# Performance work log

Hardware: AMD Instinct MI355X
Metric: run time of the kernel (lower is better)

## Reference

```python
import jax, jax.numpy as jnp
import numpy as np
import math

B, NQ, C = 8, 1024, 256
H, D = 8, 32            # heads, head_dim
L, P = 3, 8             # levels, points
FF = 1024
SHAPES = ((128, 128), (64, 64), (32, 32))   # (H_l, W_l) per level
STARTS = (0, 16384, 20480)
S = 21504


def _layernorm(x, w, b):
    m = x.mean(-1, keepdims=True)
    v = ((x - m) ** 2).mean(-1, keepdims=True)
    return (x - m) * jax.lax.rsqrt(v + 1e-5) * w + b


def _mha(x, in_w, in_b, out_w, out_b):
    # torch nn.MultiheadAttention self-attention, batch_first, eval (no dropout)
    qkv = x @ in_w.T + in_b                         # [B,Nq,3C]
    q, k, v = jnp.split(qkv, 3, axis=-1)
    q = q.reshape(B, NQ, H, D)
    k = k.reshape(B, NQ, H, D)
    v = v.reshape(B, NQ, H, D)
    scores = jnp.einsum('bqhd,bkhd->bhqk', q, k) / math.sqrt(D)
    attn = jax.nn.softmax(scores, axis=-1)
    o = jnp.einsum('bhqk,bkhd->bqhd', attn, v).reshape(B, NQ, C)
    return o @ out_w.T + out_b


def _msdeform(value, loc, attn_w):
    # value: [B,S,H,D]; loc: [B,Nq,H,L,P,2] in [0,1] (x,y); attn_w: [B,Nq,H,L,P]
    out = jnp.zeros((B, NQ, H, D), value.dtype)
    b_idx = jnp.arange(B)[:, None, None, None]
    h_idx = jnp.arange(H)[None, None, :, None]
    for l, (h_l, w_l) in enumerate(SHAPES):
        start = STARTS[l]
        val = value[:, start:start + h_l * w_l].reshape(B, h_l, w_l, H, D)
        # grid_sample align_corners=False unnormalization of grid=loc*2-1:
        gx = loc[:, :, :, l, :, 0] * w_l - 0.5      # [B,Nq,H,P]
        gy = loc[:, :, :, l, :, 1] * h_l - 0.5
        x0 = jnp.floor(gx); y0 = jnp.floor(gy)
        lx = gx - x0;       ly = gy - y0
        x0i = x0.astype(jnp.int32); y0i = y0.astype(jnp.int32)

        def corner(yi, xi):
            valid = ((xi >= 0) & (xi < w_l) & (yi >= 0) & (yi < h_l)).astype(value.dtype)
            xc = jnp.clip(xi, 0, w_l - 1)
            yc = jnp.clip(yi, 0, h_l - 1)
            v = val[b_idx, yc, xc, h_idx]           # [B,Nq,H,P,D]
            return v * valid[..., None]

        samp = (corner(y0i,     x0i)     * ((1 - lx) * (1 - ly))[..., None]
              + corner(y0i,     x0i + 1) * (lx * (1 - ly))[..., None]
              + corner(y0i + 1, x0i)     * ((1 - lx) * ly)[..., None]
              + corner(y0i + 1, x0i + 1) * (lx * ly)[..., None])
        out = out + (samp * attn_w[:, :, :, l, :, None]).sum(axis=3)
    return out


def _forward(tgt, memory, n1_w, n1_b, attn_in_w, attn_in_b, attn_out_w, attn_out_b,
             n2_w, n2_b, ref_w, ref_b, so_w, so_b, aw_w, aw_b, vp_w, vp_b,
             op_w, op_b, n3_w, n3_b, l1_w, l1_b, l2_w, l2_b):
    # self-attention block
    q = _layernorm(tgt, n1_w, n1_b)
    tgt = tgt + _mha(q, attn_in_w, attn_in_b, attn_out_w, attn_out_b)
    # deformable cross-attention block
    q = _layernorm(tgt, n2_w, n2_b)
    ref = jax.nn.sigmoid(q @ ref_w.T + ref_b)                                   # [B,Nq,2]
    value = (memory @ vp_w.T + vp_b).reshape(B, S, H, D)
    off = (q @ so_w.T + so_b).reshape(B, NQ, H, L, P, 2)
    aw = jax.nn.softmax((q @ aw_w.T + aw_b).reshape(B, NQ, H, L * P), axis=-1)
    aw = aw.reshape(B, NQ, H, L, P)
    normalizer = jnp.array([[w, h] for (h, w) in SHAPES], tgt.dtype)            # [L,2] (W,H)
    loc = ref[:, :, None, None, None, :] + off / normalizer[None, None, None, :, None, :]
    ca = _msdeform(value, loc, aw).reshape(B, NQ, C) @ op_w.T + op_b
    tgt = tgt + ca
    # FFN block
    q = _layernorm(tgt, n3_w, n3_b)
    ff = jax.nn.gelu(q @ l1_w.T + l1_b, approximate=False) @ l2_w.T + l2_b
    return tgt + ff


def setup_inputs() -> dict:
    key = jax.random.key(0)
    ks = jax.random.split(key, 16)
    w = lambda k, shp, s=0.02: (jax.random.normal(k, shp, jnp.float32) * s)
    # structured sampling_offsets bias (torch _reset_parameters)
    thetas = np.arange(H, dtype=np.float32) * (2.0 * math.pi / H)
    grid = np.stack([np.cos(thetas), np.sin(thetas)], -1)
    grid = grid / np.clip(np.abs(grid).max(-1, keepdims=True), 1e-6, None)
    grid = np.tile(grid.reshape(H, 1, 1, 2), (1, L, P, 1))
    grid = grid * (np.arange(P, dtype=np.float32) + 1.0).reshape(1, 1, P, 1)
    so_b = jnp.asarray(grid.reshape(-1))
    ones_c = jnp.ones((C,), jnp.float32)
    zeros_c = jnp.zeros((C,), jnp.float32)
    inp = {
        'tgt': jax.random.normal(ks[0], (B, NQ, C), jnp.float32),
        'memory': jax.random.normal(ks[1], (B, S, C), jnp.float32),
        'n1_w': ones_c, 'n1_b': zeros_c,
        'attn_in_w': w(ks[2], (3 * C, C)), 'attn_in_b': jnp.zeros((3 * C,), jnp.float32),
        'attn_out_w': w(ks[3], (C, C)), 'attn_out_b': zeros_c,
        'n2_w': ones_c, 'n2_b': zeros_c,
        'ref_w': w(ks[4], (2, C)), 'ref_b': jnp.zeros((2,), jnp.float32),
        'so_w': w(ks[5], (H * L * P * 2, C), 0.01), 'so_b': so_b,
        'aw_w': w(ks[6], (H * L * P, C)), 'aw_b': jnp.zeros((H * L * P,), jnp.float32),
        'vp_w': w(ks[7], (C, C)), 'vp_b': zeros_c,
        'op_w': w(ks[8], (C, C)), 'op_b': zeros_c,
        'n3_w': ones_c, 'n3_b': zeros_c,
        'l1_w': w(ks[9], (FF, C)), 'l1_b': jnp.zeros((FF,), jnp.float32),
        'l2_w': w(ks[10], (C, FF)), 'l2_b': zeros_c,
        'spatial_shapes': jnp.array(SHAPES, jnp.int32),
        'level_start_index': jnp.array(STARTS, jnp.int32),
    }
    return inp


def reference(tgt, memory, n1_w, n1_b, attn_in_w, attn_in_b, attn_out_w, attn_out_b,
              n2_w, n2_b, ref_w, ref_b, so_w, so_b, aw_w, aw_b, vp_w, vp_b,
              op_w, op_b, n3_w, n3_b, l1_w, l1_b, l2_w, l2_b,
              spatial_shapes, level_start_index):
    # spatial_shapes / level_start_index match the static SHAPES/STARTS constants
    return _forward(tgt, memory, n1_w, n1_b, attn_in_w, attn_in_b, attn_out_w, attn_out_b,
                    n2_w, n2_b, ref_w, ref_b, so_w, so_b, aw_w, aw_b, vp_w, vp_b,
                    op_w, op_b, n3_w, n3_b, l1_w, l1_b, l2_w, l2_b)
```

## Files before the change

### kernel.cpp

```cpp
#include <hip/hip_runtime.h>
#include <math.h>

#define NQR 1024
#define CDIM 256
#define SROWS 21504
#define ATTN_SCALE 0.17677669529663687f

typedef __attribute__((ext_vector_type(8))) short bf16x8;
typedef __attribute__((ext_vector_type(4))) float f32x4;

__device__ __forceinline__ ushort f2b(float x) {
  unsigned u = __float_as_uint(x);
  u += 0x7FFFu + ((u >> 16) & 1u);
  return (ushort)(u >> 16);
}
__device__ __forceinline__ float b2f(ushort b) {
  return __uint_as_float(((unsigned)b) << 16);
}

__global__ __launch_bounds__(256) void f2bf_kernel(
    const float* __restrict__ x, ushort* __restrict__ y) {
  int i = blockIdx.x * 256 + threadIdx.x;
  float4 v0 = ((const float4*)x)[i * 2];
  float4 v1 = ((const float4*)x)[i * 2 + 1];
  ushort4 o0, o1;
  o0.x = f2b(v0.x); o0.y = f2b(v0.y); o0.z = f2b(v0.z); o0.w = f2b(v0.w);
  o1.x = f2b(v1.x); o1.y = f2b(v1.y); o1.z = f2b(v1.z); o1.w = f2b(v1.w);
  ((ushort4*)y)[i * 2] = o0;
  ((ushort4*)y)[i * 2 + 1] = o1;
}

__global__ __launch_bounds__(256) void ln_kernel(
    const float* __restrict__ x, const float* __restrict__ w,
    const float* __restrict__ b, ushort* __restrict__ y) {
  int lane = threadIdx.x & 63;
  int row = (blockIdx.x << 2) + (threadIdx.x >> 6);
  float4 v = ((const float4*)(x + (size_t)row * CDIM))[lane];
  float s = v.x + v.y + v.z + v.w;
  float ss = v.x * v.x + v.y * v.y + v.z * v.z + v.w * v.w;
#pragma unroll
  for (int off = 32; off; off >>= 1) {
    s += __shfl_xor(s, off);
    ss += __shfl_xor(ss, off);
  }
  float m = s * (1.0f / 256.0f);
  float var = ss * (1.0f / 256.0f) - m * m;
  float r = rsqrtf(var + 1e-5f);
  float4 wv = ((const float4*)w)[lane];
  float4 bv = ((const float4*)b)[lane];
  ushort4 o;
  o.x = f2b((v.x - m) * r * wv.x + bv.x);
  o.y = f2b((v.y - m) * r * wv.y + bv.y);
  o.z = f2b((v.z - m) * r * wv.z + bv.z);
  o.w = f2b((v.w - m) * r * wv.w + bv.w);
  ((ushort4*)(y + (size_t)row * CDIM))[lane] = o;
}

template <bool GELU, bool RES, bool OUTBF>
__global__ __launch_bounds__(256) void gemm_bf16(
    const short* __restrict__ A, const short* __restrict__ W,
    const float* __restrict__ bias, const float* __restrict__ res,
    void* __restrict__ Cout, int M, int N, int K) {
  __shared__ short As[128 * 72];
  __shared__ short Bs[64 * 72];
  int t = threadIdx.x;
  int l = t & 63;
  int wave = t >> 6;
  int wm = wave >> 1, wn = wave & 1;
  int lrow = t >> 3;
  int lcol = (t & 7) << 3;
  size_t m0 = (size_t)blockIdx.x * 128;
  int n0 = blockIdx.y * 64;
  const short* Ag = A + (m0 + lrow) * K + lcol;
  const short* Wg = W + (size_t)(n0 + lrow) * K + lcol;
  f32x4 acc[4][2] = {};
  int fr = l & 15, fq = l >> 4;
  for (int k0 = 0; k0 < K; k0 += 64) {
    uint4 a0 = *(const uint4*)(Ag + k0);
    uint4 a1 = *(const uint4*)(Ag + (size_t)32 * K + k0);
    uint4 a2 = *(const uint4*)(Ag + (size_t)64 * K + k0);
    uint4 a3 = *(const uint4*)(Ag + (size_t)96 * K + k0);
    uint4 b0 = *(const uint4*)(Wg + k0);
    uint4 b1 = *(const uint4*)(Wg + (size_t)32 * K + k0);
    __syncthreads();
    *(uint4*)&As[lrow * 72 + lcol] = a0;
    *(uint4*)&As[(lrow + 32) * 72 + lcol] = a1;
    *(uint4*)&As[(lrow + 64) * 72 + lcol] = a2;
    *(uint4*)&As[(lrow + 96) * 72 + lcol] = a3;
    *(uint4*)&Bs[lrow * 72 + lcol] = b0;
    *(uint4*)&Bs[(lrow + 32) * 72 + lcol] = b1;
    __syncthreads();
#pragma unroll
    for (int kk = 0; kk < 2; kk++) {
      int kb = kk * 32 + fq * 8;
      bf16x8 af[4], bfr[2];
#pragma unroll
      for (int mi = 0; mi < 4; mi++)
        af[mi] = *(const bf16x8*)&As[(wm * 64 + mi * 16 + fr) * 72 + kb];
#pragma unroll
      for (int ni = 0; ni < 2; ni++)
        bfr[ni] = *(const bf16x8*)&Bs[(wn * 32 + ni * 16 + fr) * 72 + kb];
#pragma unroll
      for (int mi = 0; mi < 4; mi++)
#pragma unroll
        for (int ni = 0; ni < 2; ni++)
          acc[mi][ni] = __builtin_amdgcn_mfma_f32_16x16x32_bf16(
              af[mi], bfr[ni], acc[mi][ni], 0, 0, 0);
    }
  }
#pragma unroll
  for (int ni = 0; ni < 2; ni++) {
    int gcol = n0 + wn * 32 + ni * 16 + fr;
    float bv = bias[gcol];
#pragma unroll
    for (int mi = 0; mi < 4; mi++) {
#pragma unroll
      for (int j = 0; j < 4; j++) {
        size_t grow = m0 + wm * 64 + mi * 16 + fq * 4 + j;
        float v = acc[mi][ni][j] + bv;
        if (GELU) v = 0.5f * v * (1.0f + erff(v * 0.70710678118654752f));
        if (RES) v += res[grow * N + gcol];
        if (OUTBF)
          ((ushort*)Cout)[grow * N + gcol] = f2b(v);
        else
          ((float*)Cout)[grow * N + gcol] = v;
      }
    }
  }
}

__global__ __launch_bounds__(256) void attn_tiled(
    const float* __restrict__ qkv, ushort* __restrict__ o) {
  __shared__ float QsT[32][68];
  __shared__ float KsT[32][68];
  __shared__ float Vs[64][36];
  __shared__ float Ps[64][68];
  int qt = blockIdx.x;
  int bh = blockIdx.y;
  int b = bh >> 3, h = bh & 7;
  int t = threadIdx.x;
  int tx = t & 15, ty = t >> 4;
  int lr = t >> 2;
  int lc = (t & 3) << 2;

  {
    const float* qp = qkv + ((size_t)(b * NQR + qt * 64 + lr)) * 768 + h * 32;
    float4 a = *(const float4*)(qp + lc);
    float4 b4 = *(const float4*)(qp + lc + 16);
    QsT[lc + 0][lr] = a.x * ATTN_SCALE;
    QsT[lc + 1][lr] = a.y * ATTN_SCALE;
    QsT[lc + 2][lr] = a.z * ATTN_SCALE;
    QsT[lc + 3][lr] = a.w * ATTN_SCALE;
    QsT[lc + 16][lr] = b4.x * ATTN_SCALE;
    QsT[lc + 17][lr] = b4.y * ATTN_SCALE;
    QsT[lc + 18][lr] = b4.z * ATTN_SCALE;
    QsT[lc + 19][lr] = b4.w * ATTN_SCALE;
  }
  float m[4] = {-1e30f, -1e30f, -1e30f, -1e30f};
  float lsum[4] = {0.f, 0.f, 0.f, 0.f};
  float acc[4][2] = {};

  for (int kt = 0; kt < 16; kt++) {
    const float* kp = qkv + ((size_t)(b * NQR + kt * 64 + lr)) * 768 + 256 + h * 32;
    float4 k0 = *(const float4*)(kp + lc);
    float4 k1 = *(const float4*)(kp + lc + 16);
    const float* vp = kp + 256;
    float4 w0 = *(const float4*)(vp + lc);
    float4 w1 = *(const float4*)(vp + lc + 16);
    __syncthreads();
    KsT[lc + 0][lr] = k0.x;
    KsT[lc + 1][lr] = k0.y;
    KsT[lc + 2][lr] = k0.z;
    KsT[lc + 3][lr] = k0.w;
    KsT[lc + 16][lr] = k1.x;
    KsT[lc + 17][lr] = k1.y;
    KsT[lc + 18][lr] = k1.z;
    KsT[lc + 19][lr] = k1.w;
    *(float4*)&Vs[lr][lc] = w0;
    *(float4*)&Vs[lr][lc + 16] = w1;
    __syncthreads();
    float s[4][4] = {};
#pragma unroll
    for (int d = 0; d < 32; d++) {
      float4 a = *(const float4*)&QsT[d][ty << 2];
      float4 k = *(const float4*)&KsT[d][tx << 2];
      s[0][0] += a.x * k.x; s[0][1] += a.x * k.y; s[0][2] += a.x * k.z; s[0][3] += a.x * k.w;
      s[1][0] += a.y * k.x; s[1][1] += a.y * k.y; s[1][2] += a.y * k.z; s[1][3] += a.y * k.w;
      s[2][0] += a.z * k.x; s[2][1] += a.z * k.y; s[2][2] += a.z * k.z; s[2][3] += a.z * k.w;
      s[3][0] += a.w * k.x; s[3][1] += a.w * k.y; s[3][2] += a.w * k.z; s[3][3] += a.w * k.w;
    }
#pragma unroll
    for (int r = 0; r < 4; r++) {
      float mt = fmaxf(fmaxf(s[r][0], s[r][1]), fmaxf(s[r][2], s[r][3]));
      mt = fmaxf(mt, __shfl_xor(mt, 1));
      mt = fmaxf(mt, __shfl_xor(mt, 2));
      mt = fmaxf(mt, __shfl_xor(mt, 4));
      mt = fmaxf(mt, __shfl_xor(mt, 8));
      float mn = fmaxf(m[r], mt);
      float sc = __expf(m[r] - mn);
      m[r] = mn;
      float rs = 0.f;
#pragma unroll
      for (int c = 0; c < 4; c++) {
        s[r][c] = __expf(s[r][c] - mn);
        rs += s[r][c];
      }
      rs += __shfl_xor(rs, 1);
      rs += __shfl_xor(rs, 2);
      rs += __shfl_xor(rs, 4);
      rs += __shfl_xor(rs, 8);
      lsum[r] = lsum[r] * sc + rs;
      acc[r][0] *= sc;
      acc[r][1] *= sc;
      *(float4*)&Ps[(ty << 2) + r][tx << 2] = make_float4(s[r][0], s[r][1], s[r][2], s[r][3]);
    }
    __syncthreads();
#pragma unroll 4
    for (int k4 = 0; k4 < 16; k4++) {
      float pv[4][4];
#pragma unroll
      for (int r = 0; r < 4; r++) {
        float4 p4 = *(const float4*)&Ps[(ty << 2) + r][k4 << 2];
        pv[r][0] = p4.x; pv[r][1] = p4.y; pv[r][2] = p4.z; pv[r][3] = p4.w;
      }
#pragma unroll
      for (int j = 0; j < 4; j++) {
        float2 v = *(const float2*)&Vs[(k4 << 2) + j][tx << 1];
#pragma unroll
        for (int r = 0; r < 4; r++) {
          acc[r][0] += pv[r][j] * v.x;
          acc[r][1] += pv[r][j] * v.y;
        }
      }
    }
  }
  ushort* op = o + ((size_t)(b * NQR + qt * 64)) * 256 + h * 32;
#pragma unroll
  for (int r = 0; r < 4; r++) {
    float inv = 1.0f / lsum[r];
    ushort2 st;
    st.x = f2b(acc[r][0] * inv);
    st.y = f2b(acc[r][1] * inv);
    *(ushort2*)(op + (size_t)((ty << 2) + r) * 256 + (tx << 1)) = st;
  }
}

__global__ __launch_bounds__(256) void ref_kernel(
    const ushort* __restrict__ q2, const float* __restrict__ rw,
    const float* __restrict__ rb, float* __restrict__ refo) {
  int lane = threadIdx.x & 63;
  int row = (blockIdx.x << 2) + (threadIdx.x >> 6);
  ushort4 xr = ((const ushort4*)(q2 + (size_t)row * 256))[lane];
  float x0 = b2f(xr.x), x1 = b2f(xr.y), x2 = b2f(xr.z), x3 = b2f(xr.w);
  float4 w0 = ((const float4*)rw)[lane];
  float4 w1 = ((const float4*)(rw + 256))[lane];
  float d0 = x0 * w0.x + x1 * w0.y + x2 * w0.z + x3 * w0.w;
  float d1 = x0 * w1.x + x1 * w1.y + x2 * w1.z + x3 * w1.w;
#pragma unroll
  for (int off = 32; off; off >>= 1) {
    d0 += __shfl_xor(d0, off);
    d1 += __shfl_xor(d1, off);
  }
  if (lane == 0) {
    refo[row * 2 + 0] = 1.0f / (1.0f + __expf(-(d0 + rb[0])));
    refo[row * 2 + 1] = 1.0f / (1.0f + __expf(-(d1 + rb[1])));
  }
}

__global__ __launch_bounds__(256) void aw_softmax_kernel(float* __restrict__ aw) {
  int i = blockIdx.x * 256 + threadIdx.x;
  float* a = aw + (size_t)(i >> 3) * 192 + (i & 7) * 24;
  float v[24];
  float m = -1e30f;
#pragma unroll
  for (int k = 0; k < 24; k++) {
    v[k] = a[k];
    m = fmaxf(m, v[k]);
  }
  float sm = 0.f;
#pragma unroll
  for (int k = 0; k < 24; k++) {
    v[k] = __expf(v[k] - m);
    sm += v[k];
  }
  float inv = 1.0f / sm;
#pragma unroll
  for (int k = 0; k < 24; k++) a[k] = v[k] * inv;
}

__global__ __launch_bounds__(192) void msdeform_gather(
    const ushort* __restrict__ value, const float* __restrict__ ref,
    const float* __restrict__ off, const float* __restrict__ aw_n,
    float* __restrict__ lvl) {
  int q = blockIdx.x;
  int b = q >> 10;
  __shared__ float s_off[384];
  __shared__ float s_aw[192];
  int t = threadIdx.x;
#pragma unroll
  for (int i = 0; i < 3; i++) {
    int j = t + 192 * i;
    if (j < 384)
      s_off[j] = off[(size_t)q * 384 + j];
    else
      s_aw[j - 384] = aw_n[(size_t)q * 192 + (j - 384)];
  }
  __syncthreads();
  int h = t / 24;
  int rem = t - h * 24;
  int l = rem >> 3;
  int dg = rem & 7;
  int dim = (l == 0) ? 128 : ((l == 1) ? 64 : 32);
  int start = (l == 0) ? 0 : ((l == 1) ? 16384 : 20480);
  float fdim = (float)dim;
  float rx = ref[q * 2 + 0] * fdim - 0.5f;
  float ry = ref[q * 2 + 1] * fdim - 0.5f;
  const ushort* vl = value + ((size_t)b * SROWS + start) * 256 + h * 32 + dg * 4;
  int ebase = h * 24 + l * 8;
  float a0 = 0.f, a1 = 0.f, a2 = 0.f, a3 = 0.f;
#pragma unroll 2
  for (int p = 0; p < 8; p++) {
    int e = ebase + p;
    float gx = rx + s_off[e * 2];
    float gy = ry + s_off[e * 2 + 1];
    float fx = floorf(gx), fy = floorf(gy);
    int x0 = (int)fx, y0 = (int)fy;
    float lx = gx - fx, ly = gy - fy;
    float w = s_aw[e];
    bool xin0 = (x0 >= 0) & (x0 < dim);
    bool xin1 = (x0 + 1 >= 0) & (x0 + 1 < dim);
    bool yin0 = (y0 >= 0) & (y0 < dim);
    bool yin1 = (y0 + 1 >= 0) & (y0 + 1 < dim);
    ushort4 u00 = {0, 0, 0, 0}, u01 = {0, 0, 0, 0}, u10 = {0, 0, 0, 0}, u11 = {0, 0, 0, 0};
    if (yin0 && xin0) u00 = *(const ushort4*)(vl + (size_t)(y0 * dim + x0) * 256);
    if (yin0 && xin1) u01 = *(const ushort4*)(vl + (size_t)(y0 * dim + x0 + 1) * 256);
    if (yin1 && xin0) u10 = *(const ushort4*)(vl + (size_t)((y0 + 1) * dim + x0) * 256);
    if (yin1 && xin1) u11 = *(const ushort4*)(vl + (size_t)((y0 + 1) * dim + x0 + 1) * 256);
    float w00 = w * (1.f - lx) * (1.f - ly);
    float w01 = w * lx * (1.f - ly);
    float w10 = w * (1.f - lx) * ly;
    float w11 = w * lx * ly;
    a0 += b2f(u00.x) * w00 + b2f(u01.x) * w01 + b2f(u10.x) * w10 + b2f(u11.x) * w11;
    a1 += b2f(u00.y) * w00 + b2f(u01.y) * w01 + b2f(u10.y) * w10 + b2f(u11.y) * w11;
    a2 += b2f(u00.z) * w00 + b2f(u01.z) * w01 + b2f(u10.z) * w10 + b2f(u11.z) * w11;
    a3 += b2f(u00.w) * w00 + b2f(u01.w) * w01 + b2f(u10.w) * w10 + b2f(u11.w) * w11;
  }
  float4 o = make_float4(a0, a1, a2, a3);
  *(float4*)&lvl[(((size_t)q * 8 + h) * 3 + l) * 32 + dg * 4] = o;
}

__global__ __launch_bounds__(256) void msdeform_reduce(
    const float* __restrict__ lvl, ushort* __restrict__ out) {
  int t = threadIdx.x;
  int q = (blockIdx.x << 2) + (t >> 6);
  int h = (t >> 3) & 7, dg = t & 7;
  const float* p = lvl + ((size_t)q * 8 + h) * 96 + dg * 4;
  float4 x = *(const float4*)p;
  float4 y = *(const float4*)(p + 32);
  float4 z = *(const float4*)(p + 64);
  ushort4 o;
  o.x = f2b(x.x + y.x + z.x);
  o.y = f2b(x.y + y.y + z.y);
  o.z = f2b(x.z + y.z + z.z);
  o.w = f2b(x.w + y.w + z.w);
  *(ushort4*)(out + (size_t)q * 256 + h * 32 + dg * 4) = o;
}

extern "C" void kernel_launch(void* const* d_in, const int* in_sizes, int n_in,
                              void* d_out, int out_size, void* d_ws, size_t ws_size,
                              hipStream_t stream) {
  const float* tgt = (const float*)d_in[0];
  const float* memory = (const float*)d_in[1];
  const float* n1_w = (const float*)d_in[2];
  const float* n1_b = (const float*)d_in[3];
  const float* attn_in_w = (const float*)d_in[4];
  const float* attn_in_b = (const float*)d_in[5];
  const float* attn_out_w = (const float*)d_in[6];
  const float* attn_out_b = (const float*)d_in[7];
  const float* n2_w = (const float*)d_in[8];
  const float* n2_b = (const float*)d_in[9];
  const float* ref_w = (const float*)d_in[10];
  const float* ref_b = (const float*)d_in[11];
  const float* so_w = (const float*)d_in[12];
  const float* so_b = (const float*)d_in[13];
  const float* aw_w = (const float*)d_in[14];
  const float* aw_b = (const float*)d_in[15];
  const float* vp_w = (const float*)d_in[16];
  const float* vp_b = (const float*)d_in[17];
  const float* op_w = (const float*)d_in[18];
  const float* op_b = (const float*)d_in[19];
  const float* n3_w = (const float*)d_in[20];
  const float* n3_b = (const float*)d_in[21];
  const float* l1_w = (const float*)d_in[22];
  const float* l1_b = (const float*)d_in[23];
  const float* l2_w = (const float*)d_in[24];
  const float* l2_b = (const float*)d_in[25];
  float* out = (float*)d_out;

  char* base = (char*)d_ws;
  float* bufQKV = (float*)base;
  float* off_buf = (float*)(base + 25165824);
  float* aw_buf = (float*)(base + 37748736);
  float* ref_buf = (float*)(base + 44040192);
  ushort* q_bf = (ushort*)(base + 44105728);
  ushort* mha_bf = (ushort*)(base + 48300032);
  ushort* samp_bf = (ushort*)(base + 52494336);
  ushort* mem_bf = (ushort*)(base + 56688640);
  ushort* val_bf = (ushort*)(base + 144769024);
  ushort* wts = (ushort*)(base + 232849408);
  ushort* ff1_bf = (ushort*)bufQKV;
  float* lvl_buf = (float*)bufQKV;

  ushort* w_attn_in = wts;
  ushort* w_attn_out = wts + 196608;
  ushort* w_so = wts + 262144;
  ushort* w_aw = wts + 360448;
  ushort* w_vp = wts + 409600;
  ushort* w_op = wts + 475136;
  ushort* w_l1 = wts + 540672;
  ushort* w_l2 = wts + 802816;

  const int NR = 8192;

  f2bf_kernel<<<21504, 256, 0, stream>>>(memory, mem_bf);
  f2bf_kernel<<<96, 256, 0, stream>>>(attn_in_w, w_attn_in);
  f2bf_kernel<<<32, 256, 0, stream>>>(attn_out_w, w_attn_out);
  f2bf_kernel<<<48, 256, 0, stream>>>(so_w, w_so);
  f2bf_kernel<<<24, 256, 0, stream>>>(aw_w, w_aw);
  f2bf_kernel<<<32, 256, 0, stream>>>(vp_w, w_vp);
  f2bf_kernel<<<32, 256, 0, stream>>>(op_w, w_op);
  f2bf_kernel<<<128, 256, 0, stream>>>(l1_w, w_l1);
  f2bf_kernel<<<128, 256, 0, stream>>>(l2_w, w_l2);

  ln_kernel<<<NR / 4, 256, 0, stream>>>(tgt, n1_w, n1_b, q_bf);
  gemm_bf16<false, false, false><<<dim3(NR / 128, 768 / 64), 256, 0, stream>>>(
      (const short*)q_bf, (const short*)w_attn_in, attn_in_b, nullptr, bufQKV, NR, 768, 256);
  attn_tiled<<<dim3(16, 64), 256, 0, stream>>>(bufQKV, mha_bf);
  gemm_bf16<false, true, false><<<dim3(NR / 128, 256 / 64), 256, 0, stream>>>(
      (const short*)mha_bf, (const short*)w_attn_out, attn_out_b, tgt, out, NR, 256, 256);

  ln_kernel<<<NR / 4, 256, 0, stream>>>(out, n2_w, n2_b, q_bf);
  gemm_bf16<false, false, true><<<dim3(8 * SROWS / 128, 256 / 64), 256, 0, stream>>>(
      (const short*)mem_bf, (const short*)w_vp, vp_b, nullptr, val_bf, 8 * SROWS, 256, 256);
  ref_kernel<<<NR / 4, 256, 0, stream>>>(q_bf, ref_w, ref_b, ref_buf);
  gemm_bf16<false, false, false><<<dim3(NR / 128, 384 / 64), 256, 0, stream>>>(
      (const short*)q_bf, (const short*)w_so, so_b, nullptr, off_buf, NR, 384, 256);
  gemm_bf16<false, false, false><<<dim3(NR / 128, 192 / 64), 256, 0, stream>>>(
      (const short*)q_bf, (const short*)w_aw, aw_b, nullptr, aw_buf, NR, 192, 256);
  aw_softmax_kernel<<<256, 256, 0, stream>>>(aw_buf);
  msdeform_gather<<<NR, 192, 0, stream>>>(val_bf, ref_buf, off_buf, aw_buf, lvl_buf);
  msdeform_reduce<<<NR / 4, 256, 0, stream>>>(lvl_buf, samp_bf);
  gemm_bf16<false, true, false><<<dim3(NR / 128, 256 / 64), 256, 0, stream>>>(
      (const short*)samp_bf, (const short*)w_op, op_b, out, out, NR, 256, 256);

  ln_kernel<<<NR / 4, 256, 0, stream>>>(out, n3_w, n3_b, q_bf);
  gemm_bf16<true, false, true><<<dim3(NR / 128, 1024 / 64), 256, 0, stream>>>(
      (const short*)q_bf, (const short*)w_l1, l1_b, nullptr, ff1_bf, NR, 1024, 256);
  gemm_bf16<false, true, false><<<dim3(NR / 128, 256 / 64), 256, 0, stream>>>(
      (const short*)ff1_bf, (const short*)w_l2, l2_b, out, out, NR, 256, 1024);
}
```

Measured before the change: 732.8 us.

## Rewrite self-attention with bf16 MFMA and emit QKV projection in bf16

Replaces the scalar fp32 flash-attention kernel with one that computes QK^T and PV using 16x16x32 bf16 MFMA instructions. Each wave owns 16 query rows, and K and V tiles are staged in LDS, with V transposed. The QKV projection GEMM now writes bf16 instead of fp32, which halves that buffer's traffic. This moves the attention FLOPs onto matrix cores at the cost of bf16 rounding for QKV and for the probabilities.

```diff
diff --git a/kernel.cpp b/kernel.cpp
--- a/kernel.cpp
+++ b/kernel.cpp
@@ -129,119 +129,113 @@
   }
 }
 
-__global__ __launch_bounds__(256) void attn_tiled(
-    const float* __restrict__ qkv, ushort* __restrict__ o) {
-  __shared__ float QsT[32][68];
-  __shared__ float KsT[32][68];
-  __shared__ float Vs[64][36];
-  __shared__ float Ps[64][68];
-  int qt = blockIdx.x;
-  int bh = blockIdx.y;
+__global__ __launch_bounds__(256) void attn_mfma(
+    const ushort* __restrict__ qkv, ushort* __restrict__ o) {
+  __shared__ ushort Kt[64][40];
+  __shared__ ushort Vt[32][72];
+  __shared__ ushort Ps[4][16][72];
+  int qt = blockIdx.x, bh = blockIdx.y;
   int b = bh >> 3, h = bh & 7;
   int t = threadIdx.x;
-  int tx = t & 15, ty = t >> 4;
-  int lr = t >> 2;
-  int lc = (t & 3) << 2;
-
-  {
-    const float* qp = qkv + ((size_t)(b * NQR + qt * 64 + lr)) * 768 + h * 32;
-    float4 a = *(const float4*)(qp + lc);
-    float4 b4 = *(const float4*)(qp + lc + 16);
-    QsT[lc + 0][lr] = a.x * ATTN_SCALE;
-    QsT[lc + 1][lr] = a.y * ATTN_SCALE;
-    QsT[lc + 2][lr] = a.z * ATTN_SCALE;
-    QsT[lc + 3][lr] = a.w * ATTN_SCALE;
-    QsT[lc + 16][lr] = b4.x * ATTN_SCALE;
-    QsT[lc + 17][lr] = b4.y * ATTN_SCALE;
-    QsT[lc + 18][lr] = b4.z * ATTN_SCALE;
-    QsT[lc + 19][lr] = b4.w * ATTN_SCALE;
-  }
-  float m[4] = {-1e30f, -1e30f, -1e30f, -1e30f};
+  int w = t >> 6, l = t & 63;
+  int fr = l & 15, fg = l >> 4;
+
+  const ushort* qp =
+      qkv + ((size_t)(b * NQR + qt * 64 + w * 16 + fr)) * 768 + h * 32 + fg * 8;
+  bf16x8 qf = *(const bf16x8*)qp;
+
+  float mrow[4] = {-1e30f, -1e30f, -1e30f, -1e30f};
   float lsum[4] = {0.f, 0.f, 0.f, 0.f};
-  float acc[4][2] = {};
+  f32x4 accO[2] = {};
+
+  int rp = t & 31, vc = (t >> 5) & 3;
+  int tt = t & 127;
+  int krow = tt >> 1, kh = (tt & 1) * 16;
+
+  const ushort* kvbase = qkv + (size_t)b * NQR * 768 + 256 + h * 32;
 
   for (int kt = 0; kt < 16; kt++) {
-    const float* kp = qkv + ((size_t)(b * NQR + kt * 64 + lr)) * 768 + 256 + h * 32;
-    float4 k0 = *(const float4*)(kp + lc);
-    float4 k1 = *(const float4*)(kp + lc + 16);
-    const float* vp = kp + 256;
-    float4 w0 = *(const float4*)(vp + lc);
-    float4 w1 = *(const float4*)(vp + lc + 16);
+    int k0 = kt * 64;
+    uint4 ld0, ld1;
+    if (t < 128) {
+      const ushort* vp = kvbase + 256 + (size_t)(k0 + 2 * rp) * 768 + vc * 8;
+      ld0 = *(const uint4*)vp;
+      ld1 = *(const uint4*)(vp + 768);
+    } else {
+      const ushort* kp = kvbase + (size_t)(k0 + krow) * 768 + kh;
+      ld0 = *(const uint4*)kp;
+      ld1 = *(const uint4*)(kp + 8);
+    }
     __syncthreads();
-    KsT[lc + 0][lr] = k0.x;
-    KsT[lc + 1][lr] = k0.y;
-    KsT[lc + 2][lr] = k0.z;
-    KsT[lc + 3][lr] = k0.w;
-    KsT[lc + 16][lr] = k1.x;
-    KsT[lc + 17][lr] = k1.y;
-    KsT[lc + 18][lr] = k1.z;
-    KsT[lc + 19][lr] = k1.w;
-    *(float4*)&Vs[lr][lc] = w0;
-    *(float4*)&Vs[lr][lc + 16] = w1;
+    if (t < 128) {
+      ushort va[8], vb[8];
+      *(uint4*)va = ld0;
+      *(uint4*)vb = ld1;
+#pragma unroll
+      for (int j = 0; j < 8; j++) {
+        unsigned pack = (unsigned)va[j] | ((unsigned)vb[j] << 16);
+        *(unsigned*)&Vt[vc * 8 + j][2 * rp] = pack;
+      }
+    } else {
+      *(uint4*)&Kt[krow][kh] = ld0;
+      *(uint4*)&Kt[krow][kh + 8] = ld1;
+    }
     __syncthreads();
-    float s[4][4] = {};
-#pragma unroll
-    for (int d = 0; d < 32; d++) {
-      float4 a = *(const float4*)&QsT[d][ty << 2];
-      float4 k = *(const float4*)&KsT[d][tx << 2];
-      s[0][0] += a.x * k.x; s[0][1] += a.x * k.y; s[0][2] += a.x * k.z; s[0][3] += a.x * k.w;
-      s[1][0] += a.y * k.x; s[1][1] += a.y * k.y; s[1][2] += a.y * k.z; s[1][3] += a.y * k.w;
-      s[2][0] += a.z * k.x; s[2][1] += a.z * k.y; s[2][2] += a.z * k.z; s[2][3] += a.z * k.w;
-      s[3][0] += a.w * k.x; s[3][1] += a.w * k.y; s[3][2] += a.w * k.z; s[3][3] += a.w * k.w;
-    }
-#pragma unroll
-    for (int r = 0; r < 4; r++) {
-      float mt = fmaxf(fmaxf(s[r][0], s[r][1]), fmaxf(s[r][2], s[r][3]));
+    f32x4 sf[4];
+#pragma unroll
+    for (int nt = 0; nt < 4; nt++) {
+      bf16x8 kf = *(const bf16x8*)&Kt[nt * 16 + fr][fg * 8];
+      f32x4 z = {0.f, 0.f, 0.f, 0.f};
+      sf[nt] = __builtin_amdgcn_mfma_f32_16x16x32_bf16(qf, kf, z, 0, 0, 0);
+    }
+#pragma unroll
+    for (int j = 0; j < 4; j++) {
+      float s0 = sf[0][j] * ATTN_SCALE;
+      float s1 = sf[1][j] * ATTN_SCALE;
+      float s2 = sf[2][j] * ATTN_SCALE;
+      float s3 = sf[3][j] * ATTN_SCALE;
+      float mt = fmaxf(fmaxf(s0, s1), fmaxf(s2, s3));
       mt = fmaxf(mt, __shfl_xor(mt, 1));
       mt = fmaxf(mt, __shfl_xor(mt, 2));
       mt = fmaxf(mt, __shfl_xor(mt, 4));
       mt = fmaxf(mt, __shfl_xor(mt, 8));
-      float mn = fmaxf(m[r], mt);
-      float sc = __expf(m[r] - mn);
-      m[r] = mn;
-      float rs = 0.f;
-#pragma unroll
-      for (int c = 0; c < 4; c++) {
-        s[r][c] = __expf(s[r][c] - mn);
-        rs += s[r][c];
-      }
+      float mn = fmaxf(mrow[j], mt);
+      float scl = __expf(mrow[j] - mn);
+      mrow[j] = mn;
+      float p0 = __expf(s0 - mn), p1 = __expf(s1 - mn);
+      float p2 = __expf(s2 - mn), p3 = __expf(s3 - mn);
+      float rs = p0 + p1 + p2 + p3;
       rs += __shfl_xor(rs, 1);
       rs += __shfl_xor(rs, 2);
       rs += __shfl_xor(rs, 4);
       rs += __shfl_xor(rs, 8);
-      lsum[r] = lsum[r] * sc + rs;
-      acc[r][0] *= sc;
-      acc[r][1] *= sc;
-      *(float4*)&Ps[(ty << 2) + r][tx << 2] = make_float4(s[r][0], s[r][1], s[r][2], s[r][3]);
-    }
-    __syncthreads();
-#pragma unroll 4
-    for (int k4 = 0; k4 < 16; k4++) {
-      float pv[4][4];
-#pragma unroll
-      for (int r = 0; r < 4; r++) {
-        float4 p4 = *(const float4*)&Ps[(ty << 2) + r][k4 << 2];
-        pv[r][0] = p4.x; pv[r][1] = p4.y; pv[r][2] = p4.z; pv[r][3] = p4.w;
+      lsum[j] = lsum[j] * scl + rs;
+      accO[0][j] *= scl;
+      accO[1][j] *= scl;
+      int lq = fg * 4 + j;
+      Ps[w][lq][fr] = f2b(p0);
+      Ps[w][lq][16 + fr] = f2b(p1);
+      Ps[w][lq][32 + fr] = f2b(p2);
+      Ps[w][lq][48 + fr] = f2b(p3);
+    }
+#pragma unroll
+    for (int kk = 0; kk < 2; kk++) {
+      bf16x8 pf = *(const bf16x8*)&Ps[w][fr][kk * 32 + fg * 8];
+#pragma unroll
+      for (int nt = 0; nt < 2; nt++) {
+        bf16x8 vf = *(const bf16x8*)&Vt[nt * 16 + fr][kk * 32 + fg * 8];
+        accO[nt] = __builtin_amdgcn_mfma_f32_16x16x32_bf16(pf, vf, accO[nt], 0, 0, 0);
       }
-#pragma unroll
-      for (int j = 0; j < 4; j++) {
-        float2 v = *(const float2*)&Vs[(k4 << 2) + j][tx << 1];
-#pragma unroll
-        for (int r = 0; r < 4; r++) {
-          acc[r][0] += pv[r][j] * v.x;
-          acc[r][1] += pv[r][j] * v.y;
-        }
-      }
-    }
-  }
-  ushort* op = o + ((size_t)(b * NQR + qt * 64)) * 256 + h * 32;
-#pragma unroll
-  for (int r = 0; r < 4; r++) {
-    float inv = 1.0f / lsum[r];
-    ushort2 st;
-    st.x = f2b(acc[r][0] * inv);
-    st.y = f2b(acc[r][1] * inv);
-    *(ushort2*)(op + (size_t)((ty << 2) + r) * 256 + (tx << 1)) = st;
+    }
+  }
+  ushort* op = o + ((size_t)(b * NQR + qt * 64 + w * 16)) * 256 + h * 32;
+#pragma unroll
+  for (int j = 0; j < 4; j++) {
+    float inv = 1.0f / lsum[j];
+    int lq = fg * 4 + j;
+#pragma unroll
+    for (int nt = 0; nt < 2; nt++)
+      op[(size_t)lq * 256 + nt * 16 + fr] = f2b(accO[nt][j] * inv);
   }
 }
 
@@ -398,7 +392,7 @@
   float* out = (float*)d_out;
 
   char* base = (char*)d_ws;
-  float* bufQKV = (float*)base;
+  ushort* qkv_bf = (ushort*)base;
   float* off_buf = (float*)(base + 25165824);
   float* aw_buf = (float*)(base + 37748736);
   float* ref_buf = (float*)(base + 44040192);
@@ -408,8 +402,8 @@
   ushort* mem_bf = (ushort*)(base + 56688640);
   ushort* val_bf = (ushort*)(base + 144769024);
   ushort* wts = (ushort*)(base + 232849408);
-  ushort* ff1_bf = (ushort*)bufQKV;
-  float* lvl_buf = (float*)bufQKV;
+  ushort* ff1_bf = (ushort*)base;
+  float* lvl_buf = (float*)base;
 
   ushort* w_attn_in = wts;
   ushort* w_attn_out = wts + 196608;
@@ -433,9 +427,9 @@
   f2bf_kernel<<<128, 256, 0, stream>>>(l2_w, w_l2);
 
   ln_kernel<<<NR / 4, 256, 0, stream>>>(tgt, n1_w, n1_b, q_bf);
-  gemm_bf16<false, false, false><<<dim3(NR / 128, 768 / 64), 256, 0, stream>>>(
-      (const short*)q_bf, (const short*)w_attn_in, attn_in_b, nullptr, bufQKV, NR, 768, 256);
-  attn_tiled<<<dim3(16, 64), 256, 0, stream>>>(bufQKV, mha_bf);
+  gemm_bf16<false, false, true><<<dim3(NR / 128, 768 / 64), 256, 0, stream>>>(
+      (const short*)q_bf, (const short*)w_attn_in, attn_in_b, nullptr, qkv_bf, NR, 768, 256);
+  attn_mfma<<<dim3(16, 64), 256, 0, stream>>>(qkv_bf, mha_bf);
   gemm_bf16<false, true, false><<<dim3(NR / 128, 256 / 64), 256, 0, stream>>>(
       (const short*)mha_bf, (const short*)w_attn_out, attn_out_b, tgt, out, NR, 256, 256);
 
```

New measurement: 589.8 us. 1.24x faster.
